# Performance work log

Hardware: AMD Instinct MI355X
Metric: run time of the kernel (lower is better)

## Reference

```python
import jax, jax.numpy as jnp
import numpy as np

WINDOW = 7
HEADS = 4
HEAD_DIM = 32
DISP = WINDOW // 2  # shifted displacement = 3
SCALE = HEADS ** (-0.5)  # faithful to source (heads, not head_dim)


def _create_mask(ws, d, upper_lower, left_right):
    m = np.zeros((ws * ws, ws * ws), dtype=np.float32)
    if upper_lower:
        m[-d * ws:, :-d * ws] = -np.inf
        m[:-d * ws, -d * ws:] = -np.inf
    if left_right:
        m = m.reshape(ws, ws, ws, ws)
        m[:, -d:, :, :-d] = -np.inf
        m[:, :-d, :, -d:] = -np.inf
        m = m.reshape(ws * ws, ws * ws)
    return m


def _relative_indices(ws):
    coords = np.array([[x, y] for x in range(ws) for y in range(ws)])
    return (coords[None, :, :] - coords[:, None, :]) + ws - 1  # (ws^2, ws^2, 2)


def setup_inputs() -> dict:
    key = jax.random.key(0)
    k1, k2, k3, k4 = jax.random.split(key, 4)
    inner = HEADS * HEAD_DIM
    return {
        "x": jax.random.normal(k1, (64, 56, 56, 128), dtype=jnp.float32),
        "w_qkv": jax.random.normal(k2, (3 * inner, 128), dtype=jnp.float32) * 0.02,
        "pos_embedding": jax.random.normal(k3, (2 * WINDOW - 1, 2 * WINDOW - 1), dtype=jnp.float32),
        "w_out": jax.random.normal(k4, (128, inner), dtype=jnp.float32) * 0.02,
        "b_out": jnp.zeros((128,), dtype=jnp.float32),
    }


def _to_windows(t, ws, heads, hd):
    b, H, W, _ = t.shape
    nwh, nww = H // ws, W // ws
    t = t.reshape(b, nwh, ws, nww, ws, heads, hd)
    # -> (b, h, nw, ws^2, d)
    return t.transpose(0, 5, 1, 3, 2, 4, 6).reshape(b, heads, nwh * nww, ws * ws, hd)


def _from_windows(t, ws, nwh, nww):
    b, h, nw, s2, d = t.shape
    t = t.reshape(b, h, nwh, nww, ws, ws, d)
    # -> (b, H, W, h*d)
    return t.transpose(0, 2, 4, 3, 5, 1, 6).reshape(b, nwh * ws, nww * ws, h * d)


def reference(x, w_qkv, pos_embedding, w_out, b_out):
    ws = WINDOW
    b, H, W, _ = x.shape
    nwh, nww = H // ws, W // ws

    # cyclic shift
    x = jnp.roll(x, shift=(-DISP, -DISP), axis=(1, 2))

    qkv = x @ w_qkv.T  # (b,H,W,3*inner)
    q, k, v = jnp.split(qkv, 3, axis=-1)
    q = _to_windows(q, ws, HEADS, HEAD_DIM)
    k = _to_windows(k, ws, HEADS, HEAD_DIM)
    v = _to_windows(v, ws, HEADS, HEAD_DIM)

    scores = jnp.einsum('bhwid,bhwjd->bhwij', q, k) * SCALE

    # relative position bias gather
    ri = _relative_indices(ws)
    bias = pos_embedding[ri[:, :, 0], ri[:, :, 1]]  # (ws^2, ws^2)
    scores = scores + bias

    # shift masks added only to specific window rows/columns
    ul = _create_mask(ws, DISP, True, False)
    lr = _create_mask(ws, DISP, False, True)
    full_mask = np.zeros((nwh * nww, ws * ws, ws * ws), dtype=np.float32)
    full_mask[-nww:] += ul
    full_mask[nww - 1::nww] += lr
    scores = scores + jnp.asarray(full_mask)

    probs = jax.nn.softmax(scores, axis=-1)
    attn = jnp.einsum('bhwij,bhwjd->bhwid', probs, v)

    out = _from_windows(attn, ws, nwh, nww)
    out = out @ w_out.T + b_out
    out = jnp.roll(out, shift=(DISP, DISP), axis=(1, 2))
    return out
```

## Files before the change

kernel.cpp:

```cpp
#include <hip/hip_runtime.h>

#define IMG 56
#define CH  128
#define S2  49
#define DSP 3
#define MTS 50
#define MVS 2500

#define LDA   128
#define LDQK  256
#define LDP   64
#define LDVT  56
#define OFF_U 25088
#define SMEM_BYTES 39440

typedef __attribute__((ext_vector_type(8))) short bf16x8;
typedef __attribute__((ext_vector_type(4))) float f32x4;

__device__ __forceinline__ unsigned short f2bs(float f) {
    unsigned u = __float_as_uint(f);
    return (unsigned short)((u + 0x7fffu + ((u >> 16) & 1u)) >> 16);
}

__device__ __forceinline__ int idxA2(int row, int col) {
    int blk = (col >> 3) ^ (row & 7);
    return row * LDA + blk * 8 + (col & 7);
}
__device__ __forceinline__ int idxQK(int row, int col) {
    int blk = (col >> 3) ^ (row & 7);
    return row * LDQK + blk * 8 + (col & 7);
}

__global__ __launch_bounds__(256)
void swin_prep(const float* __restrict__ w_qkv,
               const float* __restrict__ w_out,
               const float* __restrict__ pe,
               unsigned short* __restrict__ wqb,
               unsigned short* __restrict__ wob,
               float* __restrict__ mt4)
{
    const int tid = (int)(blockIdx.x * blockDim.x + threadIdx.x);
    const int np  = (int)(gridDim.x * blockDim.x);
    for (int i = tid; i < 384 * CH; i += np) wqb[i] = f2bs(w_qkv[i]);
    for (int i = tid; i < CH * CH;  i += np) wob[i] = f2bs(w_out[i]);
    for (int i = tid; i < 4 * S2 * S2; i += np) {
        const int v  = i / (S2 * S2), r = i - v * (S2 * S2);
        const int ii = r / S2, jj = r - ii * S2;
        const int iy = ii / 7, ix = ii - iy * 7;
        const int jy = jj / 7, jx = jj - jy * 7;
        float val = pe[(jy - iy + 6) * 13 + (jx - ix + 6)];
        if ((v & 2) && ((iy >= 4) != (jy >= 4))) val = -1e30f;
        if ((v & 1) && ((ix >= 4) != (jx >= 4))) val = -1e30f;
        mt4[v * MVS + ii * MTS + jj] = val;
    }
}

__global__ __launch_bounds__(256, 4)
void swin_fused(const float* __restrict__ x,
                const unsigned short* __restrict__ wqb,
                const float* __restrict__ mt4,
                const unsigned short* __restrict__ wob,
                const float* __restrict__ b_out,
                float* __restrict__ out)
{
    __shared__ __align__(16) char smem[SMEM_BYTES];
    unsigned short* const ldsQK = (unsigned short*)smem;
    unsigned short* const ldsU  = (unsigned short*)(smem + OFF_U);

    const int tid  = (int)threadIdx.x;
    const int wave = tid >> 6, lane = tid & 63;
    const int lm   = lane & 15, lq = lane >> 4;
    const int b    = (int)blockIdx.y;
    const int wh   = (int)blockIdx.x >> 3, ww = (int)blockIdx.x & 7;
    const bool my  = (wh == 7), mx = (ww == 7);
    const float* const mtg = mt4 + (((my ? 2 : 0) + (mx ? 1 : 0)) * MVS);

    if (tid < 2) ((unsigned long long*)(smem + OFF_U + 2 * (size_t)CH * LDVT))[tid] = 0ull;
    for (int idx = tid; idx < S2 * 32; idx += 256) {
        const int s  = idx >> 5, c4 = (idx & 31) << 2;
        const int iy = s / 7, ix = s - iy * 7;
        int gy = wh * 7 + iy + DSP; if (gy >= IMG) gy -= IMG;
        int gx = ww * 7 + ix + DSP; if (gx >= IMG) gx -= IMG;
        const float4 v = *(const float4*)(x + (size_t)((b * IMG + gy) * IMG + gx) * CH + c4);
        uint2 p;
        p.x = (unsigned)f2bs(v.x) | ((unsigned)f2bs(v.y) << 16);
        p.y = (unsigned)f2bs(v.z) | ((unsigned)f2bs(v.w) << 16);
        *(uint2*)(ldsU + idxA2(s, c4)) = p;
    }
    __syncthreads();

    {
        bf16x8 af[4][4];
        #pragma unroll
        for (int mt = 0; mt < 4; ++mt) {
            const int row = (mt < 3) ? (mt * 16 + lm) : 48;
            #pragma unroll
            for (int kt = 0; kt < 4; ++kt)
                af[mt][kt] = *(const bf16x8*)(ldsU + idxA2(row, kt * 32 + lq * 8));
        }
        __syncthreads();

        #pragma unroll
        for (int nt = 0; nt < 6; ++nt) {
            const int n0 = (wave * 6 + nt) * 16;
            const unsigned short* wb = wqb + (size_t)(n0 + lm) * CH + lq * 8;
            bf16x8 bf[4];
            #pragma unroll
            for (int kt = 0; kt < 4; ++kt)
                bf[kt] = *(const bf16x8*)(wb + kt * 32);
            f32x4 c0 = {0.f,0.f,0.f,0.f}, c1 = {0.f,0.f,0.f,0.f};
            f32x4 c2 = {0.f,0.f,0.f,0.f}, c3 = {0.f,0.f,0.f,0.f};
            #pragma unroll
            for (int kt = 0; kt < 4; ++kt) {
                c0 = __builtin_amdgcn_mfma_f32_16x16x32_bf16(af[0][kt], bf[kt], c0, 0, 0, 0);
                c1 = __builtin_amdgcn_mfma_f32_16x16x32_bf16(af[1][kt], bf[kt], c1, 0, 0, 0);
                c2 = __builtin_amdgcn_mfma_f32_16x16x32_bf16(af[2][kt], bf[kt], c2, 0, 0, 0);
                c3 = __builtin_amdgcn_mfma_f32_16x16x32_bf16(af[3][kt], bf[kt], c3, 0, 0, 0);
            }
            const int col = n0 + lm;
            if (n0 < 256) {
                #pragma unroll
                for (int mt = 0; mt < 4; ++mt) {
                    const f32x4 c = (mt == 0) ? c0 : (mt == 1) ? c1 : (mt == 2) ? c2 : c3;
                    const int rb = mt * 16 + lq * 4;
                    #pragma unroll
                    for (int r = 0; r < 4; ++r) {
                        const int row = rb + r;
                        if (row < S2) ldsQK[idxQK(row, col)] = f2bs(c[r]);
                    }
                }
            } else {
                const int d = col - 256;
                #pragma unroll
                for (int mt = 0; mt < 4; ++mt) {
                    const f32x4 c = (mt == 0) ? c0 : (mt == 1) ? c1 : (mt == 2) ? c2 : c3;
                    const int rb = mt * 16 + lq * 4;
                    if (rb < LDVT) {
                        unsigned long long pk = 0;
                        #pragma unroll
                        for (int r = 0; r < 4; ++r) {
                            const unsigned short us = (rb + r < S2) ? f2bs(c[r]) : (unsigned short)0;
                            pk |= (unsigned long long)us << (16 * r);
                        }
                        *(unsigned long long*)(ldsU + (size_t)d * LDVT + rb) = pk;
                    }
                }
            }
        }
    }
    __syncthreads();

    {
        const int h = wave;
        unsigned short* const ldsP = (unsigned short*)(smem + wave * 6272);

        bf16x8 qa[4], kb[4];
        #pragma unroll
        for (int mt = 0; mt < 4; ++mt)
            qa[mt] = *(const bf16x8*)(ldsQK + idxQK(mt * 16 + lm, h * 32 + lq * 8));
        #pragma unroll
        for (int nt = 0; nt < 4; ++nt)
            kb[nt] = *(const bf16x8*)(ldsQK + idxQK(nt * 16 + lm, CH + h * 32 + lq * 8));

        f32x4 c[4][4];
        #pragma unroll
        for (int mt = 0; mt < 4; ++mt)
            #pragma unroll
            for (int nt = 0; nt < 4; ++nt) {
                f32x4 z = {0.f, 0.f, 0.f, 0.f};
                c[mt][nt] = __builtin_amdgcn_mfma_f32_16x16x32_bf16(qa[mt], kb[nt], z, 0, 0, 0);
            }

        __syncthreads();

        bool colok[4];
        #pragma unroll
        for (int nt = 0; nt < 4; ++nt) colok[nt] = (nt * 16 + lm) < S2;

        #pragma unroll
        for (int mt = 0; mt < 4; ++mt) {
            #pragma unroll
            for (int r = 0; r < 4; ++r) {
                const int row  = mt * 16 + lq * 4 + r;
                const int rowc = row < S2 ? row : (S2 - 1);
                const float* mrow = mtg + rowc * MTS + lm;
                const float p0 = colok[0] ? __expf(c[mt][0][r] * 0.5f + mrow[0])  : 0.f;
                const float p1 = colok[1] ? __expf(c[mt][1][r] * 0.5f + mrow[16]) : 0.f;
                const float p2 = colok[2] ? __expf(c[mt][2][r] * 0.5f + mrow[32]) : 0.f;
                const float p3 = colok[3] ? __expf(c[mt][3][r] * 0.5f + mrow[48]) : 0.f;
                float ll = (p0 + p1) + (p2 + p3);
                ll += __shfl_xor(ll, 1);
                ll += __shfl_xor(ll, 2);
                ll += __shfl_xor(ll, 4);
                ll += __shfl_xor(ll, 8);
                const float inv = 1.0f / ll;
                c[mt][0][r] = p0 * inv; c[mt][1][r] = p1 * inv;
                c[mt][2][r] = p2 * inv; c[mt][3][r] = p3 * inv;
            }
        }

        #pragma unroll
        for (int mt = 0; mt < 4; ++mt)
            #pragma unroll
            for (int r = 0; r < 4; ++r) {
                const int row = mt * 16 + lq * 4 + r;
                if (row < S2) {
                    #pragma unroll
                    for (int nt = 0; nt < 4; ++nt) {
                        const int col = nt * 16 + lm;
                        const int blk = (col >> 3) ^ (row & 7);
                        ldsP[row * LDP + blk * 8 + (col & 7)] = f2bs(c[mt][nt][r]);
                    }
                }
            }

        bf16x8 pa[4][2], vb[2][2];
        #pragma unroll
        for (int mt = 0; mt < 4; ++mt) {
            const int row = mt * 16 + lm;
            #pragma unroll
            for (int kt = 0; kt < 2; ++kt) {
                const int blk = (kt * 4 + lq) ^ (row & 7);
                pa[mt][kt] = *(const bf16x8*)(ldsP + row * LDP + blk * 8);
            }
        }
        #pragma unroll
        for (int nt = 0; nt < 2; ++nt) {
            const int d = h * 32 + nt * 16 + lm;
            #pragma unroll
            for (int kt = 0; kt < 2; ++kt)
                vb[nt][kt] = *(const bf16x8*)(ldsU + (size_t)d * LDVT + kt * 32 + lq * 8);
        }
        __syncthreads();

        f32x4 oc[4][2];
        #pragma unroll
        for (int mt = 0; mt < 4; ++mt)
            #pragma unroll
            for (int nt = 0; nt < 2; ++nt) {
                f32x4 z = {0.f, 0.f, 0.f, 0.f};
                z = __builtin_amdgcn_mfma_f32_16x16x32_bf16(pa[mt][0], vb[nt][0], z, 0, 0, 0);
                oc[mt][nt] = __builtin_amdgcn_mfma_f32_16x16x32_bf16(pa[mt][1], vb[nt][1], z, 0, 0, 0);
            }

        #pragma unroll
        for (int mt = 0; mt < 4; ++mt)
            #pragma unroll
            for (int r = 0; r < 4; ++r) {
                const int row = mt * 16 + lq * 4 + r;
                if (row < S2) {
                    #pragma unroll
                    for (int nt = 0; nt < 2; ++nt)
                        ldsU[idxA2(row, h * 32 + nt * 16 + lm)] = f2bs(oc[mt][nt][r]);
                }
            }
    }
    __syncthreads();

    {
        bf16x8 af[4][4];
        #pragma unroll
        for (int mt = 0; mt < 4; ++mt) {
            const int row = (mt < 3) ? (mt * 16 + lm) : 48;
            #pragma unroll
            for (int kt = 0; kt < 4; ++kt)
                af[mt][kt] = *(const bf16x8*)(ldsU + idxA2(row, kt * 32 + lq * 8));
        }

        #pragma unroll
        for (int nt = 0; nt < 2; ++nt) {
            const int n0 = (wave * 2 + nt) * 16;
            const unsigned short* wb = wob + (size_t)(n0 + lm) * CH + lq * 8;
            bf16x8 bf[4];
            #pragma unroll
            for (int kt = 0; kt < 4; ++kt)
                bf[kt] = *(const bf16x8*)(wb + kt * 32);
            f32x4 c0 = {0.f,0.f,0.f,0.f}, c1 = {0.f,0.f,0.f,0.f};
            f32x4 c2 = {0.f,0.f,0.f,0.f}, c3 = {0.f,0.f,0.f,0.f};
            #pragma unroll
            for (int kt = 0; kt < 4; ++kt) {
                c0 = __builtin_amdgcn_mfma_f32_16x16x32_bf16(af[0][kt], bf[kt], c0, 0, 0, 0);
                c1 = __builtin_amdgcn_mfma_f32_16x16x32_bf16(af[1][kt], bf[kt], c1, 0, 0, 0);
                c2 = __builtin_amdgcn_mfma_f32_16x16x32_bf16(af[2][kt], bf[kt], c2, 0, 0, 0);
                c3 = __builtin_amdgcn_mfma_f32_16x16x32_bf16(af[3][kt], bf[kt], c3, 0, 0, 0);
            }
            const int col = n0 + lm;
            const float bo = b_out[col];
            #pragma unroll
            for (int mt = 0; mt < 4; ++mt) {
                const f32x4 c = (mt == 0) ? c0 : (mt == 1) ? c1 : (mt == 2) ? c2 : c3;
                const int rb = mt * 16 + lq * 4;
                #pragma unroll
                for (int r = 0; r < 4; ++r) {
                    const int s = rb + r;
                    if (s < S2) {
                        const int sy = s / 7, sx = s - sy * 7;
                        int gy = wh * 7 + sy + DSP; if (gy >= IMG) gy -= IMG;
                        int gx = ww * 7 + sx + DSP; if (gx >= IMG) gx -= IMG;
                        out[(size_t)((b * IMG + gy) * IMG + gx) * CH + col] = c[r] + bo;
                    }
                }
            }
        }
    }
}

extern "C" void kernel_launch(void* const* d_in, const int* in_sizes, int n_in,
                              void* d_out, int out_size, void* d_ws, size_t ws_size,
                              hipStream_t stream) {
    const float* x      = (const float*)d_in[0];
    const float* w_qkv  = (const float*)d_in[1];
    const float* pe     = (const float*)d_in[2];
    const float* w_out  = (const float*)d_in[3];
    const float* b_out  = (const float*)d_in[4];
    float* out = (float*)d_out;

    unsigned short* wqb = (unsigned short*)d_ws;
    unsigned short* wob = (unsigned short*)((char*)d_ws + 98304);
    float*          mt4 = (float*)((char*)d_ws + 131072);

    swin_prep<<<dim3(128), 256, 0, stream>>>(w_qkv, w_out, pe, wqb, wob, mt4);

    dim3 grid(64, 64);
    swin_fused<<<grid, 256, 0, stream>>>(x, wqb, mt4, wob, b_out, out);
}
```

Measured before the change: 298.6 us.

## Prefetch inputs, weights and mask into registers; use packed bf16 conversions

Loads the x tile and the first QKV weight fragments into registers before any LDS writes, and prefetches the next weight tiles, mask rows and output-projection weights ahead of use. The goal is to hide global-memory latency behind computation. It also replaces the software bf16 rounding with the v_cvt_pk_bf16_f32 instruction, raises wave priority around the MFMA blocks, and merges the output-projection phase into the attention scope. The cost is higher register pressure, which may lower occupancy.

```diff
diff --git a/kernel.cpp b/kernel.cpp
--- a/kernel.cpp
+++ b/kernel.cpp
@@ -20,6 +20,12 @@
 __device__ __forceinline__ unsigned short f2bs(float f) {
     unsigned u = __float_as_uint(f);
     return (unsigned short)((u + 0x7fffu + ((u >> 16) & 1u)) >> 16);
+}
+
+__device__ __forceinline__ unsigned cvtpk(float lo, float hi) {
+    unsigned r;
+    asm("v_cvt_pk_bf16_f32 %0, %1, %2" : "=v"(r) : "v"(lo), "v"(hi));
+    return r;
 }
 
 __device__ __forceinline__ int idxA2(int row, int col) {
@@ -75,17 +81,36 @@
     const bool my  = (wh == 7), mx = (ww == 7);
     const float* const mtg = mt4 + (((my ? 2 : 0) + (mx ? 1 : 0)) * MVS);
 
+    float4 xv[7];
+    #pragma unroll
+    for (int p = 0; p < 7; ++p) {
+        if (p < 6 || tid < 32) {
+            const int idx = tid + p * 256;
+            const int s  = idx >> 5, c4 = (idx & 31) << 2;
+            const int iy = s / 7, ix = s - iy * 7;
+            int gy = wh * 7 + iy + DSP; if (gy >= IMG) gy -= IMG;
+            int gx = ww * 7 + ix + DSP; if (gx >= IMG) gx -= IMG;
+            xv[p] = *(const float4*)(x + (size_t)((b * IMG + gy) * IMG + gx) * CH + c4);
+        }
+    }
+    bf16x8 wr[6][4];
+    #pragma unroll
+    for (int nt = 0; nt < 2; ++nt) {
+        const unsigned short* wb = wqb + (size_t)((wave * 6 + nt) * 16 + lm) * CH + lq * 8;
+        #pragma unroll
+        for (int kt = 0; kt < 4; ++kt) wr[nt][kt] = *(const bf16x8*)(wb + kt * 32);
+    }
     if (tid < 2) ((unsigned long long*)(smem + OFF_U + 2 * (size_t)CH * LDVT))[tid] = 0ull;
-    for (int idx = tid; idx < S2 * 32; idx += 256) {
-        const int s  = idx >> 5, c4 = (idx & 31) << 2;
-        const int iy = s / 7, ix = s - iy * 7;
-        int gy = wh * 7 + iy + DSP; if (gy >= IMG) gy -= IMG;
-        int gx = ww * 7 + ix + DSP; if (gx >= IMG) gx -= IMG;
-        const float4 v = *(const float4*)(x + (size_t)((b * IMG + gy) * IMG + gx) * CH + c4);
-        uint2 p;
-        p.x = (unsigned)f2bs(v.x) | ((unsigned)f2bs(v.y) << 16);
-        p.y = (unsigned)f2bs(v.z) | ((unsigned)f2bs(v.w) << 16);
-        *(uint2*)(ldsU + idxA2(s, c4)) = p;
+    #pragma unroll
+    for (int p = 0; p < 7; ++p) {
+        if (p < 6 || tid < 32) {
+            const int idx = tid + p * 256;
+            const int s  = idx >> 5, c4 = (idx & 31) << 2;
+            uint2 pk;
+            pk.x = cvtpk(xv[p].x, xv[p].y);
+            pk.y = cvtpk(xv[p].z, xv[p].w);
+            *(uint2*)(ldsU + idxA2(s, c4)) = pk;
+        }
     }
     __syncthreads();
 
@@ -102,21 +127,21 @@
 
         #pragma unroll
         for (int nt = 0; nt < 6; ++nt) {
-            const int n0 = (wave * 6 + nt) * 16;
-            const unsigned short* wb = wqb + (size_t)(n0 + lm) * CH + lq * 8;
-            bf16x8 bf[4];
-            #pragma unroll
-            for (int kt = 0; kt < 4; ++kt)
-                bf[kt] = *(const bf16x8*)(wb + kt * 32);
+            if (nt < 4) {
+                const unsigned short* wb = wqb + (size_t)((wave * 6 + nt + 2) * 16 + lm) * CH + lq * 8;
+                #pragma unroll
+                for (int kt = 0; kt < 4; ++kt) wr[nt + 2][kt] = *(const bf16x8*)(wb + kt * 32);
+            }
             f32x4 c0 = {0.f,0.f,0.f,0.f}, c1 = {0.f,0.f,0.f,0.f};
             f32x4 c2 = {0.f,0.f,0.f,0.f}, c3 = {0.f,0.f,0.f,0.f};
             #pragma unroll
             for (int kt = 0; kt < 4; ++kt) {
-                c0 = __builtin_amdgcn_mfma_f32_16x16x32_bf16(af[0][kt], bf[kt], c0, 0, 0, 0);
-                c1 = __builtin_amdgcn_mfma_f32_16x16x32_bf16(af[1][kt], bf[kt], c1, 0, 0, 0);
-                c2 = __builtin_amdgcn_mfma_f32_16x16x32_bf16(af[2][kt], bf[kt], c2, 0, 0, 0);
-                c3 = __builtin_amdgcn_mfma_f32_16x16x32_bf16(af[3][kt], bf[kt], c3, 0, 0, 0);
-            }
+                c0 = __builtin_amdgcn_mfma_f32_16x16x32_bf16(af[0][kt], wr[nt][kt], c0, 0, 0, 0);
+                c1 = __builtin_amdgcn_mfma_f32_16x16x32_bf16(af[1][kt], wr[nt][kt], c1, 0, 0, 0);
+                c2 = __builtin_amdgcn_mfma_f32_16x16x32_bf16(af[2][kt], wr[nt][kt], c2, 0, 0, 0);
+                c3 = __builtin_amdgcn_mfma_f32_16x16x32_bf16(af[3][kt], wr[nt][kt], c3, 0, 0, 0);
+            }
+            const int n0  = (wave * 6 + nt) * 16;
             const int col = n0 + lm;
             if (n0 < 256) {
                 #pragma unroll
@@ -124,9 +149,11 @@
                     const f32x4 c = (mt == 0) ? c0 : (mt == 1) ? c1 : (mt == 2) ? c2 : c3;
                     const int rb = mt * 16 + lq * 4;
                     #pragma unroll
-                    for (int r = 0; r < 4; ++r) {
-                        const int row = rb + r;
-                        if (row < S2) ldsQK[idxQK(row, col)] = f2bs(c[r]);
+                    for (int rp = 0; rp < 2; ++rp) {
+                        const unsigned pk = cvtpk(c[2 * rp], c[2 * rp + 1]);
+                        const int row0 = rb + 2 * rp;
+                        if (row0 < S2)     ldsQK[idxQK(row0, col)]     = (unsigned short)pk;
+                        if (row0 + 1 < S2) ldsQK[idxQK(row0 + 1, col)] = (unsigned short)(pk >> 16);
                     }
                 }
             } else {
@@ -136,13 +163,13 @@
                     const f32x4 c = (mt == 0) ? c0 : (mt == 1) ? c1 : (mt == 2) ? c2 : c3;
                     const int rb = mt * 16 + lq * 4;
                     if (rb < LDVT) {
-                        unsigned long long pk = 0;
-                        #pragma unroll
-                        for (int r = 0; r < 4; ++r) {
-                            const unsigned short us = (rb + r < S2) ? f2bs(c[r]) : (unsigned short)0;
-                            pk |= (unsigned long long)us << (16 * r);
-                        }
-                        *(unsigned long long*)(ldsU + (size_t)d * LDVT + rb) = pk;
+                        const float e0 = (rb + 0 < S2) ? c[0] : 0.f;
+                        const float e1 = (rb + 1 < S2) ? c[1] : 0.f;
+                        const float e2 = (rb + 2 < S2) ? c[2] : 0.f;
+                        const float e3 = (rb + 3 < S2) ? c[3] : 0.f;
+                        const unsigned lo = cvtpk(e0, e1), hi = cvtpk(e2, e3);
+                        *(unsigned long long*)(ldsU + (size_t)d * LDVT + rb) =
+                            (unsigned long long)lo | ((unsigned long long)hi << 32);
                     }
                 }
             }
@@ -162,7 +189,21 @@
         for (int nt = 0; nt < 4; ++nt)
             kb[nt] = *(const bf16x8*)(ldsQK + idxQK(nt * 16 + lm, CH + h * 32 + lq * 8));
 
+        float mk[4][4][4];
+        auto loadmk = [&](float (&dst)[4][4], int mtv) {
+            #pragma unroll
+            for (int r = 0; r < 4; ++r) {
+                const int row  = mtv * 16 + lq * 4 + r;
+                const int rowc = row < S2 ? row : (S2 - 1);
+                const float* mrow = mtg + rowc * MTS + lm;
+                #pragma unroll
+                for (int nt = 0; nt < 4; ++nt) dst[r][nt] = mrow[nt * 16];
+            }
+        };
+        loadmk(mk[0], 0);
+
         f32x4 c[4][4];
+        __builtin_amdgcn_s_setprio(1);
         #pragma unroll
         for (int mt = 0; mt < 4; ++mt)
             #pragma unroll
@@ -170,6 +211,7 @@
                 f32x4 z = {0.f, 0.f, 0.f, 0.f};
                 c[mt][nt] = __builtin_amdgcn_mfma_f32_16x16x32_bf16(qa[mt], kb[nt], z, 0, 0, 0);
             }
+        __builtin_amdgcn_s_setprio(0);
 
         __syncthreads();
 
@@ -179,15 +221,13 @@
 
         #pragma unroll
         for (int mt = 0; mt < 4; ++mt) {
+            if (mt < 3) loadmk(mk[mt + 1], mt + 1);
             #pragma unroll
             for (int r = 0; r < 4; ++r) {
-                const int row  = mt * 16 + lq * 4 + r;
-                const int rowc = row < S2 ? row : (S2 - 1);
-                const float* mrow = mtg + rowc * MTS + lm;
-                const float p0 = colok[0] ? __expf(c[mt][0][r] * 0.5f + mrow[0])  : 0.f;
-                const float p1 = colok[1] ? __expf(c[mt][1][r] * 0.5f + mrow[16]) : 0.f;
-                const float p2 = colok[2] ? __expf(c[mt][2][r] * 0.5f + mrow[32]) : 0.f;
-                const float p3 = colok[3] ? __expf(c[mt][3][r] * 0.5f + mrow[48]) : 0.f;
+                const float p0 = colok[0] ? __expf(c[mt][0][r] * 0.5f + mk[mt][r][0]) : 0.f;
+                const float p1 = colok[1] ? __expf(c[mt][1][r] * 0.5f + mk[mt][r][1]) : 0.f;
+                const float p2 = colok[2] ? __expf(c[mt][2][r] * 0.5f + mk[mt][r][2]) : 0.f;
+                const float p3 = colok[3] ? __expf(c[mt][3][r] * 0.5f + mk[mt][r][3]) : 0.f;
                 float ll = (p0 + p1) + (p2 + p3);
                 ll += __shfl_xor(ll, 1);
                 ll += __shfl_xor(ll, 2);
@@ -202,14 +242,19 @@
         #pragma unroll
         for (int mt = 0; mt < 4; ++mt)
             #pragma unroll
-            for (int r = 0; r < 4; ++r) {
-                const int row = mt * 16 + lq * 4 + r;
-                if (row < S2) {
-                    #pragma unroll
-                    for (int nt = 0; nt < 4; ++nt) {
-                        const int col = nt * 16 + lm;
-                        const int blk = (col >> 3) ^ (row & 7);
-                        ldsP[row * LDP + blk * 8 + (col & 7)] = f2bs(c[mt][nt][r]);
+            for (int nt = 0; nt < 4; ++nt) {
+                const int col = nt * 16 + lm;
+                #pragma unroll
+                for (int rp = 0; rp < 2; ++rp) {
+                    const unsigned pk = cvtpk(c[mt][nt][2 * rp], c[mt][nt][2 * rp + 1]);
+                    const int row0 = mt * 16 + lq * 4 + 2 * rp;
+                    if (row0 < S2) {
+                        const int blk = (col >> 3) ^ (row0 & 7);
+                        ldsP[row0 * LDP + blk * 8 + (col & 7)] = (unsigned short)pk;
+                    }
+                    if (row0 + 1 < S2) {
+                        const int blk = (col >> 3) ^ ((row0 + 1) & 7);
+                        ldsP[(row0 + 1) * LDP + blk * 8 + (col & 7)] = (unsigned short)(pk >> 16);
                     }
                 }
             }
@@ -231,9 +276,19 @@
             for (int kt = 0; kt < 2; ++kt)
                 vb[nt][kt] = *(const bf16x8*)(ldsU + (size_t)d * LDVT + kt * 32 + lq * 8);
         }
+        bf16x8 wo[2][4];
+        #pragma unroll
+        for (int nt = 0; nt < 2; ++nt) {
+            const unsigned short* wb = wob + (size_t)((wave * 2 + nt) * 16 + lm) * CH + lq * 8;
+            #pragma unroll
+            for (int kt = 0; kt < 4; ++kt) wo[nt][kt] = *(const bf16x8*)(wb + kt * 32);
+        }
+        const float bo0 = b_out[wave * 32 + lm];
+        const float bo1 = b_out[wave * 32 + 16 + lm];
         __syncthreads();
 
         f32x4 oc[4][2];
+        __builtin_amdgcn_s_setprio(1);
         #pragma unroll
         for (int mt = 0; mt < 4; ++mt)
             #pragma unroll
@@ -242,22 +297,23 @@
                 z = __builtin_amdgcn_mfma_f32_16x16x32_bf16(pa[mt][0], vb[nt][0], z, 0, 0, 0);
                 oc[mt][nt] = __builtin_amdgcn_mfma_f32_16x16x32_bf16(pa[mt][1], vb[nt][1], z, 0, 0, 0);
             }
-
-        #pragma unroll
-        for (int mt = 0; mt < 4; ++mt)
-            #pragma unroll
-            for (int r = 0; r < 4; ++r) {
-                const int row = mt * 16 + lq * 4 + r;
-                if (row < S2) {
-                    #pragma unroll
-                    for (int nt = 0; nt < 2; ++nt)
-                        ldsU[idxA2(row, h * 32 + nt * 16 + lm)] = f2bs(oc[mt][nt][r]);
-                }
-            }
-    }
-    __syncthreads();
-
-    {
+        __builtin_amdgcn_s_setprio(0);
+
+        #pragma unroll
+        for (int mt = 0; mt < 4; ++mt)
+            #pragma unroll
+            for (int nt = 0; nt < 2; ++nt) {
+                const int col = h * 32 + nt * 16 + lm;
+                #pragma unroll
+                for (int rp = 0; rp < 2; ++rp) {
+                    const unsigned pk = cvtpk(oc[mt][nt][2 * rp], oc[mt][nt][2 * rp + 1]);
+                    const int row0 = mt * 16 + lq * 4 + 2 * rp;
+                    if (row0 < S2)     ldsU[idxA2(row0, col)]     = (unsigned short)pk;
+                    if (row0 + 1 < S2) ldsU[idxA2(row0 + 1, col)] = (unsigned short)(pk >> 16);
+                }
+            }
+        __syncthreads();
+
         bf16x8 af[4][4];
         #pragma unroll
         for (int mt = 0; mt < 4; ++mt) {
@@ -267,41 +323,33 @@
                 af[mt][kt] = *(const bf16x8*)(ldsU + idxA2(row, kt * 32 + lq * 8));
         }
 
-        #pragma unroll
-        for (int nt = 0; nt < 2; ++nt) {
-            const int n0 = (wave * 2 + nt) * 16;
-            const unsigned short* wb = wob + (size_t)(n0 + lm) * CH + lq * 8;
-            bf16x8 bf[4];
-            #pragma unroll
-            for (int kt = 0; kt < 4; ++kt)
-                bf[kt] = *(const bf16x8*)(wb + kt * 32);
-            f32x4 c0 = {0.f,0.f,0.f,0.f}, c1 = {0.f,0.f,0.f,0.f};
-            f32x4 c2 = {0.f,0.f,0.f,0.f}, c3 = {0.f,0.f,0.f,0.f};
-            #pragma unroll
-            for (int kt = 0; kt < 4; ++kt) {
-                c0 = __builtin_amdgcn_mfma_f32_16x16x32_bf16(af[0][kt], bf[kt], c0, 0, 0, 0);
-                c1 = __builtin_amdgcn_mfma_f32_16x16x32_bf16(af[1][kt], bf[kt], c1, 0, 0, 0);
-                c2 = __builtin_amdgcn_mfma_f32_16x16x32_bf16(af[2][kt], bf[kt], c2, 0, 0, 0);
-                c3 = __builtin_amdgcn_mfma_f32_16x16x32_bf16(af[3][kt], bf[kt], c3, 0, 0, 0);
-            }
-            const int col = n0 + lm;
-            const float bo = b_out[col];
+        f32x4 d[2][4];
+        #pragma unroll
+        for (int nt = 0; nt < 2; ++nt)
             #pragma unroll
             for (int mt = 0; mt < 4; ++mt) {
-                const f32x4 c = (mt == 0) ? c0 : (mt == 1) ? c1 : (mt == 2) ? c2 : c3;
-                const int rb = mt * 16 + lq * 4;
-                #pragma unroll
-                for (int r = 0; r < 4; ++r) {
-                    const int s = rb + r;
-                    if (s < S2) {
-                        const int sy = s / 7, sx = s - sy * 7;
-                        int gy = wh * 7 + sy + DSP; if (gy >= IMG) gy -= IMG;
-                        int gx = ww * 7 + sx + DSP; if (gx >= IMG) gx -= IMG;
-                        out[(size_t)((b * IMG + gy) * IMG + gx) * CH + col] = c[r] + bo;
-                    }
-                }
-            }
-        }
+                f32x4 acc = {0.f,0.f,0.f,0.f};
+                #pragma unroll
+                for (int kt = 0; kt < 4; ++kt)
+                    acc = __builtin_amdgcn_mfma_f32_16x16x32_bf16(af[mt][kt], wo[nt][kt], acc, 0, 0, 0);
+                d[nt][mt] = acc;
+            }
+
+        const int colb = wave * 32 + lm;
+        #pragma unroll
+        for (int mt = 0; mt < 4; ++mt)
+            #pragma unroll
+            for (int r = 0; r < 4; ++r) {
+                const int s = mt * 16 + lq * 4 + r;
+                if (s < S2) {
+                    const int sy = s / 7, sx = s - sy * 7;
+                    int gy = wh * 7 + sy + DSP; if (gy >= IMG) gy -= IMG;
+                    int gx = ww * 7 + sx + DSP; if (gx >= IMG) gx -= IMG;
+                    float* op = out + (size_t)((b * IMG + gy) * IMG + gx) * CH;
+                    op[colb]      = d[0][mt][r] + bo0;
+                    op[colb + 16] = d[1][mt][r] + bo1;
+                }
+            }
     }
 }
 
```

Result: faster. 283.6 us (-5.0%).
